# Kernel optimization log

Hardware: AMD Instinct MI355X
Metric: run time of the kernel (lower is better)

The kernel has to match this reference:

```python
import jax, jax.numpy as jnp
import numpy as np
from functools import partial

T, N, E, F_IN, H, F_OUT, L = 12, 20000, 320000, 128, 256, 128, 2


def _agg(feat, src, dst, n):
    # copy_u('x','m') + sum('m','h_N'): for each dst node, sum src-node features
    return jax.ops.segment_sum(feat[src], dst, num_segments=n)


def setup_inputs() -> dict:
    key = jax.random.key(0)
    ks = jax.random.split(key, 16)
    sc = 0.05
    inp = {
        "x": jax.random.normal(ks[0], (T, N, F_IN), jnp.float32),
        "h0": jax.random.normal(ks[1], (L, N, H), jnp.float32),
        "src": jax.random.randint(ks[2], (E,), 0, N, jnp.int32),
        "dst": jax.random.randint(ks[3], (E,), 0, N, jnp.int32),
        # layer 0: x-nets map F_IN->H, h-nets map H->H; stacked [r, u, c]
        "Wx0": jax.random.normal(ks[4], (3, F_IN, H), jnp.float32) * sc,
        "bx0": jnp.zeros((3, H), jnp.float32),
        "Wh0": jax.random.normal(ks[5], (3, H, H), jnp.float32) * sc,
        "bh0": jnp.zeros((3, H), jnp.float32),
        # layer 1: both map H->H
        "Wx1": jax.random.normal(ks[6], (3, H, H), jnp.float32) * sc,
        "bx1": jnp.zeros((3, H), jnp.float32),
        "Wh1": jax.random.normal(ks[7], (3, H, H), jnp.float32) * sc,
        "bh1": jnp.zeros((3, H), jnp.float32),
        "Wo": jax.random.normal(ks[8], (H, F_OUT), jnp.float32) * sc,
        "bo": jnp.zeros((F_OUT,), jnp.float32),
    }
    return inp


def _gru_cell(x_agg, h, Wx, bx, Wh, bh, src, dst, n):
    # reuse_msg_passing=True: h_agg computed once, shared by r_h_net and u_h_net
    h_agg = _agg(h, src, dst, n)
    r = jax.nn.sigmoid(x_agg @ Wx[0] + bx[0] + h_agg @ Wh[0] + bh[0])
    u = jax.nn.sigmoid(x_agg @ Wx[1] + bx[1] + h_agg @ Wh[1] + bh[1])
    # c_h_net runs on r*h, so it needs its own aggregation
    c = jnp.tanh(x_agg @ Wx[2] + bx[2] + _agg(r * h, src, dst, n) @ Wh[2] + bh[2])
    return u * h + (1.0 - u) * c


def reference(x, h0, src, dst, Wx0, bx0, Wh0, bh0, Wx1, bx1, Wh1, bh1, Wo, bo):
    n = h0.shape[1]
    # merge_time_steps=True: aggregate all time steps of x in one pass
    x_aggs = jax.vmap(lambda xi: _agg(xi, src, dst, n))(x)  # [T, N, F_IN]

    def step(carry, x_agg_t):
        h_0, h_1 = carry
        nh0 = _gru_cell(x_agg_t, h_0, Wx0, bx0, Wh0, bh0, src, dst, n)
        nh1 = _gru_cell(_agg(nh0, src, dst, n), h_1, Wx1, bx1, Wh1, bh1, src, dst, n)
        return (nh0, nh1), nh1 @ Wo + bo

    (hf0, hf1), outputs = jax.lax.scan(step, (h0[0], h0[1]), x_aggs)
    return outputs, jnp.stack([hf0, hf1])  # [T,N,F_OUT], [L,N,H]
```

## Files before the change

### kernel.cpp

```cpp
#include <hip/hip_runtime.h>
#include <hip/hip_bf16.h>
#include <stdint.h>

#define T_STEPS 12
#define NN 20000
#define NE 320000
#define FIN 128
#define HD 256
#define FOUT 128
#define PADR 96

typedef __attribute__((ext_vector_type(4))) float f32x4;
typedef __attribute__((ext_vector_type(8))) _Float16 f16x8;

static __device__ __forceinline__ float sigmoidf_(float x) {
  return 1.0f / (1.0f + __expf(-x));
}
static __device__ __forceinline__ float tanhf_(float x) {
  return 1.0f - 2.0f / (__expf(2.0f * x) + 1.0f);
}
static __device__ __forceinline__ ushort f2h(float f) {
  union { ushort s; _Float16 h; } v; v.h = (_Float16)f; return v.s;
}

static __device__ __forceinline__ void gload_lds16(const _Float16* g, _Float16* l) {
  auto gp = (const __attribute__((address_space(1))) _Float16*)g;
  auto lp = (__attribute__((address_space(3))) _Float16*)l;
  __builtin_amdgcn_global_load_lds(gp, lp, 16, 0, 0);
}

__global__ void count_kernel(const int* __restrict__ dst, int* __restrict__ counts) {
  int e = blockIdx.x * blockDim.x + threadIdx.x;
  if (e < NE) atomicAdd(&counts[dst[e]], 1);
}

__global__ void scan_kernel(const int* __restrict__ counts, int* __restrict__ offs,
                            int* __restrict__ cursor) {
  __shared__ int sm[1024];
  __shared__ int carry_s;
  if (threadIdx.x == 0) carry_s = 0;
  __syncthreads();
  const int n = NN;
  int nch = (n + 1023) >> 10;
  for (int c = 0; c < nch; ++c) {
    int i = (c << 10) + (int)threadIdx.x;
    int v = (i < n) ? counts[i] : 0;
    sm[threadIdx.x] = v;
    __syncthreads();
    for (int off = 1; off < 1024; off <<= 1) {
      int t = (threadIdx.x >= (unsigned)off) ? sm[threadIdx.x - off] : 0;
      __syncthreads();
      sm[threadIdx.x] += t;
      __syncthreads();
    }
    int incl = sm[threadIdx.x];
    int carry_local = carry_s;
    if (i < n) {
      int excl = carry_local + incl - v;
      offs[i] = excl;
      cursor[i] = excl;
    }
    __syncthreads();
    if (threadIdx.x == 1023) carry_s = carry_local + incl;
    __syncthreads();
  }
  if (threadIdx.x == 0) offs[n] = carry_s;
}

__global__ void fill_kernel(const int* __restrict__ src, const int* __restrict__ dst,
                            int* __restrict__ cursor, int* __restrict__ esrc) {
  int e = blockIdx.x * blockDim.x + threadIdx.x;
  if (e < NE) {
    int d = dst[e];
    int pos = atomicAdd(&cursor[d], 1);
    esrc[pos] = src[e];
  }
}

static __device__ __forceinline__ void agg_body256(int blk, const float* __restrict__ feat,
                                                   const int* __restrict__ offs,
                                                   const int* __restrict__ esrc,
                                                   _Float16* __restrict__ out) {
  int d = blk * 4 + (threadIdx.x >> 6);
  int lane = threadIdx.x & 63;
  int beg = offs[d], end = offs[d + 1];
  float a[8][4] = {};
  int e = beg;
  for (; e + 7 < end; e += 8) {
    int s[8];
#pragma unroll
    for (int u = 0; u < 8; ++u) s[u] = __builtin_amdgcn_readfirstlane(esrc[e + u]);
#pragma unroll
    for (int u = 0; u < 8; ++u) {
      float4 v = *reinterpret_cast<const float4*>(feat + (size_t)s[u] * 256 + lane * 4);
      a[u][0] += v.x; a[u][1] += v.y; a[u][2] += v.z; a[u][3] += v.w;
    }
  }
  for (; e + 3 < end; e += 4) {
    int s[4];
#pragma unroll
    for (int u = 0; u < 4; ++u) s[u] = __builtin_amdgcn_readfirstlane(esrc[e + u]);
#pragma unroll
    for (int u = 0; u < 4; ++u) {
      float4 v = *reinterpret_cast<const float4*>(feat + (size_t)s[u] * 256 + lane * 4);
      a[u][0] += v.x; a[u][1] += v.y; a[u][2] += v.z; a[u][3] += v.w;
    }
  }
  for (; e < end; ++e) {
    int s0 = __builtin_amdgcn_readfirstlane(esrc[e]);
    float4 v = *reinterpret_cast<const float4*>(feat + (size_t)s0 * 256 + lane * 4);
    a[0][0] += v.x; a[0][1] += v.y; a[0][2] += v.z; a[0][3] += v.w;
  }
  ushort hi[4], lo[4];
#pragma unroll
  for (int p = 0; p < 4; ++p) {
    float s = ((a[0][p] + a[1][p]) + (a[2][p] + a[3][p])) +
              ((a[4][p] + a[5][p]) + (a[6][p] + a[7][p]));
    hi[p] = f2h(s);
    union { ushort us; _Float16 h; } u; u.us = hi[p];
    lo[p] = f2h(s - (float)u.h);
  }
  *reinterpret_cast<ushort4*>(out + (size_t)d * 512 + lane * 4) = *reinterpret_cast<ushort4*>(hi);
  *reinterpret_cast<ushort4*>(out + (size_t)d * 512 + 256 + lane * 4) = *reinterpret_cast<ushort4*>(lo);
}

__global__ void agg_split_h(const float* __restrict__ feat, const int* __restrict__ offs,
                            const int* __restrict__ esrc, _Float16* __restrict__ out) {
  agg_body256(blockIdx.x, feat, offs, esrc, out);
}

__global__ void agg_dual(const float* __restrict__ f0, _Float16* __restrict__ o0,
                         const float* __restrict__ f1, _Float16* __restrict__ o1,
                         const int* __restrict__ offs, const int* __restrict__ esrc) {
  if (blockIdx.y == 0) agg_body256(blockIdx.x, f0, offs, esrc, o0);
  else                 agg_body256(blockIdx.x, f1, offs, esrc, o1);
}

__global__ void agg_split_x(const float* __restrict__ x, const int* __restrict__ offs,
                            const int* __restrict__ esrc, _Float16* __restrict__ out) {
  int t = blockIdx.y;
  const float* feat = x + (size_t)t * NN * FIN;
  _Float16* o = out + (size_t)t * NN * 256;
  int d = blockIdx.x * 4 + (threadIdx.x >> 6);
  int lane = threadIdx.x & 63;
  int beg = offs[d], end = offs[d + 1];
  float a[8][2] = {};
  int e = beg;
  for (; e + 7 < end; e += 8) {
    int s[8];
#pragma unroll
    for (int u = 0; u < 8; ++u) s[u] = __builtin_amdgcn_readfirstlane(esrc[e + u]);
#pragma unroll
    for (int u = 0; u < 8; ++u) {
      float2 v = *reinterpret_cast<const float2*>(feat + (size_t)s[u] * FIN + lane * 2);
      a[u][0] += v.x; a[u][1] += v.y;
    }
  }
  for (; e + 3 < end; e += 4) {
    int s[4];
#pragma unroll
    for (int u = 0; u < 4; ++u) s[u] = __builtin_amdgcn_readfirstlane(esrc[e + u]);
#pragma unroll
    for (int u = 0; u < 4; ++u) {
      float2 v = *reinterpret_cast<const float2*>(feat + (size_t)s[u] * FIN + lane * 2);
      a[u][0] += v.x; a[u][1] += v.y;
    }
  }
  for (; e < end; ++e) {
    int s0 = __builtin_amdgcn_readfirstlane(esrc[e]);
    float2 v = *reinterpret_cast<const float2*>(feat + (size_t)s0 * FIN + lane * 2);
    a[0][0] += v.x; a[0][1] += v.y;
  }
  float s0 = ((a[0][0] + a[1][0]) + (a[2][0] + a[3][0])) +
             ((a[4][0] + a[5][0]) + (a[6][0] + a[7][0]));
  float s1 = ((a[0][1] + a[1][1]) + (a[2][1] + a[3][1])) +
             ((a[4][1] + a[5][1]) + (a[6][1] + a[7][1]));
  ushort2 hi, lo;
  hi.x = f2h(s0); hi.y = f2h(s1);
  union { ushort s; _Float16 h; } u0, u1;
  u0.s = hi.x; u1.s = hi.y;
  lo.x = f2h(s0 - (float)u0.h); lo.y = f2h(s1 - (float)u1.h);
  *reinterpret_cast<ushort2*>(o + (size_t)d * 256 + lane * 2) = hi;
  *reinterpret_cast<ushort2*>(o + (size_t)d * 256 + FIN + lane * 2) = lo;
}

struct GemmP {
  const _Float16* Aa; int lda_a, wrapA, lenA;
  const _Float16* Ab; int lda_b, wrapB;
  const _Float16* B; int ldb;
  float* C; int ldc;
  const float* bias;
  const float* Cacc;
  int M, K, mode;
  float* h; _Float16* hf; float* rh;
  int nch, rpg;
};

static __device__ __forceinline__ void gemm_body(int p, const GemmP& g,
                                                 _Float16* As, _Float16* Bs) {
  int xcd = p & 7;
  int q = p >> 3;
  int rowt = xcd * g.rpg + q / g.nch;
  int chunk = q % g.nch;
  int m0 = rowt * 128;
  if (m0 >= g.M) return;
  int n0 = chunk * 128;

  int tid = threadIdx.x;
  int wave = tid >> 6;
  int lane = tid & 63;
  int wm = wave >> 1, wn = wave & 1;
  int lrow = lane & 15;
  int kgrp = lane >> 4;

  f32x4 acc[4][4] = {};

  int row8 = lane >> 3;
  int swz8 = 8 * ((lane & 7) ^ row8);
  int wrow = wave * 32;

  for (int k0 = 0; k0 < g.K; k0 += 64) {
    const _Float16* Abase;
    int ka, ldA;
    if (k0 < g.lenA) {
      ka = (k0 >= g.wrapA) ? k0 - g.wrapA : k0;
      Abase = g.Aa; ldA = g.lda_a;
    } else {
      int kp = k0 - g.lenA;
      ka = (kp >= g.wrapB) ? kp - g.wrapB : kp;
      Abase = g.Ab; ldA = g.lda_b;
    }
    __syncthreads();
#pragma unroll
    for (int p4 = 0; p4 < 4; ++p4) {
      int r = wrow + p4 * 8;
      gload_lds16(&Abase[(size_t)(m0 + r + row8) * ldA + ka + swz8], &As[r * 64]);
      gload_lds16(&g.B[(size_t)(n0 + r + row8) * g.ldb + k0 + swz8], &Bs[r * 64]);
    }
    __syncthreads();

#pragma unroll
    for (int kk = 0; kk < 2; ++kk) {
      f16x8 af[4], bf[4];
      int kbyte = kk * 64 + kgrp * 16;
#pragma unroll
      for (int i = 0; i < 4; ++i) {
        int ar = wm * 64 + i * 16 + lrow;
        af[i] = *reinterpret_cast<const f16x8*>(
            reinterpret_cast<const char*>(As) + ar * 128 + (kbyte ^ ((ar & 7) << 4)));
        int br = wn * 64 + i * 16 + lrow;
        bf[i] = *reinterpret_cast<const f16x8*>(
            reinterpret_cast<const char*>(Bs) + br * 128 + (kbyte ^ ((br & 7) << 4)));
      }
#pragma unroll
      for (int i = 0; i < 4; ++i)
#pragma unroll
        for (int j = 0; j < 4; ++j)
          acc[i][j] = __builtin_amdgcn_mfma_f32_16x16x32_f16(bf[j], af[i], acc[i][j], 0, 0, 0);
    }
  }

#pragma unroll
  for (int i = 0; i < 4; ++i) {
    int m = m0 + wm * 64 + i * 16 + lrow;
    if (m >= g.M) continue;
#pragma unroll
    for (int j = 0; j < 4; ++j) {
      int colbase = n0 + wn * 64 + j * 16 + kgrp * 4;
      f32x4 v = acc[i][j];
      if (g.mode == 0) {
        float4 bv4 = *reinterpret_cast<const float4*>(&g.bias[colbase]);
        v[0] += bv4.x; v[1] += bv4.y; v[2] += bv4.z; v[3] += bv4.w;
        *reinterpret_cast<f32x4*>(&g.C[(size_t)m * g.ldc + colbase]) = v;
      } else if (g.mode == 1) {
        if (g.Cacc) {
          float4 a4 = *reinterpret_cast<const float4*>(&g.Cacc[(size_t)m * g.ldc + colbase]);
          v[0] += a4.x; v[1] += a4.y; v[2] += a4.z; v[3] += a4.w;
        } else {
          float4 bv4 = *reinterpret_cast<const float4*>(&g.bias[colbase]);
          v[0] += bv4.x; v[1] += bv4.y; v[2] += bv4.z; v[3] += bv4.w;
        }
        if (colbase < 256) {
          float4 hv = *reinterpret_cast<const float4*>(&g.h[(size_t)m * 256 + colbase]);
          f32x4 rv;
          rv[0] = sigmoidf_(v[0]) * hv.x;
          rv[1] = sigmoidf_(v[1]) * hv.y;
          rv[2] = sigmoidf_(v[2]) * hv.z;
          rv[3] = sigmoidf_(v[3]) * hv.w;
          *reinterpret_cast<f32x4*>(&g.rh[(size_t)m * 256 + colbase]) = rv;
        } else if (colbase < 512) {
          v[0] = sigmoidf_(v[0]); v[1] = sigmoidf_(v[1]);
          v[2] = sigmoidf_(v[2]); v[3] = sigmoidf_(v[3]);
          *reinterpret_cast<f32x4*>(&g.C[(size_t)m * g.ldc + colbase]) = v;
        } else {
          *reinterpret_cast<f32x4*>(&g.C[(size_t)m * g.ldc + colbase]) = v;
        }
      } else {
        float4 xc = *reinterpret_cast<const float4*>(&g.C[(size_t)m * g.ldc + 512 + colbase]);
        float4 uu = *reinterpret_cast<const float4*>(&g.C[(size_t)m * g.ldc + 256 + colbase]);
        float* hp = &g.h[(size_t)m * 256 + colbase];
        float4 hv = *reinterpret_cast<const float4*>(hp);
        float4 nh;
        nh.x = uu.x * hv.x + (1.f - uu.x) * tanhf_(xc.x + v[0]);
        nh.y = uu.y * hv.y + (1.f - uu.y) * tanhf_(xc.y + v[1]);
        nh.z = uu.z * hv.z + (1.f - uu.z) * tanhf_(xc.z + v[2]);
        nh.w = uu.w * hv.w + (1.f - uu.w) * tanhf_(xc.w + v[3]);
        *reinterpret_cast<float4*>(hp) = nh;
        if (g.hf) {
          ushort4 hv16;
          hv16.x = f2h(nh.x); hv16.y = f2h(nh.y);
          hv16.z = f2h(nh.z); hv16.w = f2h(nh.w);
          *reinterpret_cast<ushort4*>(&g.hf[(size_t)m * 256 + colbase]) = hv16;
        }
      }
    }
  }
}

__global__ __launch_bounds__(256) void combo(GemmP ga, int na, GemmP gb, int nb, GemmP gc) {
  __shared__ _Float16 As[128 * 64];
  __shared__ _Float16 Bs[128 * 64];
  int b = blockIdx.x;
  int sel = (b < na) ? 0 : ((b < na + nb) ? 1 : 2);
  int idx = b - ((sel > 0) ? na : 0) - ((sel > 1) ? nb : 0);
  GemmP g = (sel == 0) ? ga : ((sel == 1) ? gb : gc);
  gemm_body(idx, g, As, Bs);
}

__global__ void wtrans(const float* __restrict__ W, _Float16* __restrict__ dst,
                       int K, int ldw, int ldd, int koff, int mode) {
  int k = blockIdx.x * blockDim.x + threadIdx.x;
  int n = blockIdx.y;
  if (k < K) {
    float w = W[(size_t)k * ldw + n];
    _Float16 hi = (_Float16)w;
    dst[(size_t)n * ldd + koff + k] = mode ? (_Float16)(w - (float)hi) : hi;
  }
}

__global__ void bias_comb(const float* __restrict__ bx, const float* __restrict__ bh,
                          float* __restrict__ out) {
  int i = blockIdx.x * blockDim.x + threadIdx.x;
  if (i < 768) out[i] = bx[i] + bh[i];
}

__global__ void copy_kernel(const float* __restrict__ in, float* __restrict__ out, int n4) {
  int i = blockIdx.x * blockDim.x + threadIdx.x;
  if (i < n4) reinterpret_cast<float4*>(out)[i] = reinterpret_cast<const float4*>(in)[i];
}

extern "C" void kernel_launch(void* const* d_in, const int* in_sizes, int n_in,
                              void* d_out, int out_size, void* d_ws, size_t ws_size,
                              hipStream_t stream) {
  const float* x   = (const float*)d_in[0];
  const float* h0  = (const float*)d_in[1];
  const int*   src = (const int*)d_in[2];
  const int*   dst = (const int*)d_in[3];
  const float* Wx0 = (const float*)d_in[4];
  const float* bx0 = (const float*)d_in[5];
  const float* Wh0 = (const float*)d_in[6];
  const float* bh0 = (const float*)d_in[7];
  const float* Wx1 = (const float*)d_in[8];
  const float* bx1 = (const float*)d_in[9];
  const float* Wh1 = (const float*)d_in[10];
  const float* bh1 = (const float*)d_in[11];
  const float* Wo  = (const float*)d_in[12];
  const float* bo  = (const float*)d_in[13];
  float* out = (float*)d_out;

  char* p = (char*)d_ws;
  auto alloc = [&](size_t bytes) {
    char* r = p;
    p += (bytes + 255) & ~(size_t)255;
    return r;
  };
  int* offs   = (int*)alloc((NN + 1) * sizeof(int));
  int* cursor = (int*)alloc(NN * sizeof(int));
  int* counts = (int*)alloc(NN * sizeof(int));
  int* esrc   = (int*)alloc(NE * sizeof(int));
  _Float16* B0  = (_Float16*)alloc((size_t)768 * 1152 * 2);
  _Float16* B0h = (_Float16*)alloc((size_t)256 * 768 * 2);
  _Float16* B1  = (_Float16*)alloc((size_t)768 * 1536 * 2);
  _Float16* B1h = (_Float16*)alloc((size_t)256 * 768 * 2);
  _Float16* Bo  = (_Float16*)alloc((size_t)128 * 256 * 2);
  float* b0c  = (float*)alloc(768 * 4);
  float* b1c  = (float*)alloc(768 * 4);
  _Float16* XAGG  = (_Float16*)alloc(((size_t)T_STEPS * NN + PADR) * 256 * 2);
  _Float16* H0AGG = (_Float16*)alloc((size_t)(NN + PADR) * 512 * 2);
  _Float16* H1AGG = (_Float16*)alloc((size_t)(NN + PADR) * 512 * 2);
  _Float16* RHAGG = (_Float16*)alloc((size_t)(NN + PADR) * 512 * 2);
  _Float16* h1f   = (_Float16*)alloc((size_t)(NN + PADR) * 256 * 2);
  float* rhf  = (float*)alloc((size_t)NN * 256 * 4);
  float* xw0  = (float*)alloc((size_t)NN * 768 * 4);
  float* xw1  = (float*)alloc((size_t)NN * 768 * 4);

  float* h0c = out + (size_t)T_STEPS * NN * FOUT;
  float* h1c = h0c + (size_t)NN * HD;

  hipMemsetAsync(counts, 0, NN * sizeof(int), stream);
  count_kernel<<<(NE + 255) / 256, 256, 0, stream>>>(dst, counts);
  scan_kernel<<<1, 1024, 0, stream>>>(counts, offs, cursor);
  fill_kernel<<<(NE + 255) / 256, 256, 0, stream>>>(src, dst, cursor, esrc);

  hipMemsetAsync(B0, 0, (size_t)768 * 1152 * 2, stream);
  hipMemsetAsync(B1, 0, (size_t)768 * 1536 * 2, stream);
  for (int g = 0; g < 3; ++g) {
    const float* W = Wx0 + (size_t)g * 128 * 256;
    _Float16* D = B0 + (size_t)g * 256 * 1152;
    wtrans<<<dim3(1, 256), 256, 0, stream>>>(W, D, 128, 256, 1152, 0, 0);
    wtrans<<<dim3(1, 256), 256, 0, stream>>>(W, D, 128, 256, 1152, 128, 0);
    wtrans<<<dim3(1, 256), 256, 0, stream>>>(W, D, 128, 256, 1152, 256, 1);
  }
  for (int g = 0; g < 2; ++g) {
    const float* W = Wh0 + (size_t)g * 256 * 256;
    _Float16* D = B0 + (size_t)g * 256 * 1152;
    wtrans<<<dim3(1, 256), 256, 0, stream>>>(W, D, 256, 256, 1152, 384, 0);
    wtrans<<<dim3(1, 256), 256, 0, stream>>>(W, D, 256, 256, 1152, 640, 0);
    wtrans<<<dim3(1, 256), 256, 0, stream>>>(W, D, 256, 256, 1152, 896, 1);
  }
  {
    const float* W = Wh0 + (size_t)2 * 256 * 256;
    wtrans<<<dim3(1, 256), 256, 0, stream>>>(W, B0h, 256, 256, 768, 0, 0);
    wtrans<<<dim3(1, 256), 256, 0, stream>>>(W, B0h, 256, 256, 768, 256, 0);
    wtrans<<<dim3(1, 256), 256, 0, stream>>>(W, B0h, 256, 256, 768, 512, 1);
  }
  for (int g = 0; g < 3; ++g) {
    const float* W = Wx1 + (size_t)g * 256 * 256;
    _Float16* D = B1 + (size_t)g * 256 * 1536;
    wtrans<<<dim3(1, 256), 256, 0, stream>>>(W, D, 256, 256, 1536, 0, 0);
    wtrans<<<dim3(1, 256), 256, 0, stream>>>(W, D, 256, 256, 1536, 256, 0);
    wtrans<<<dim3(1, 256), 256, 0, stream>>>(W, D, 256, 256, 1536, 512, 1);
  }
  for (int g = 0; g < 2; ++g) {
    const float* W = Wh1 + (size_t)g * 256 * 256;
    _Float16* D = B1 + (size_t)g * 256 * 1536;
    wtrans<<<dim3(1, 256), 256, 0, stream>>>(W, D, 256, 256, 1536, 768, 0);
    wtrans<<<dim3(1, 256), 256, 0, stream>>>(W, D, 256, 256, 1536, 1024, 0);
    wtrans<<<dim3(1, 256), 256, 0, stream>>>(W, D, 256, 256, 1536, 1280, 1);
  }
  {
    const float* W = Wh1 + (size_t)2 * 256 * 256;
    wtrans<<<dim3(1, 256), 256, 0, stream>>>(W, B1h, 256, 256, 768, 0, 0);
    wtrans<<<dim3(1, 256), 256, 0, stream>>>(W, B1h, 256, 256, 768, 256, 0);
    wtrans<<<dim3(1, 256), 256, 0, stream>>>(W, B1h, 256, 256, 768, 512, 1);
  }
  wtrans<<<dim3(1, 128), 256, 0, stream>>>(Wo, Bo, 256, 128, 256, 0, 0);
  bias_comb<<<3, 256, 0, stream>>>(bx0, bh0, b0c);
  bias_comb<<<3, 256, 0, stream>>>(bx1, bh1, b1c);

  copy_kernel<<<(2 * NN * HD / 4 + 255) / 256, 256, 0, stream>>>(h0, h0c, 2 * NN * HD / 4);

  dim3 blk(256);
  const int RPG = 20;
  int g6 = 8 * RPG * 6, g2 = 8 * RPG * 2, g1 = 8 * RPG * 1;
  int agg_grid = NN / 4;

  agg_split_x<<<dim3(agg_grid, T_STEPS), blk, 0, stream>>>(x, offs, esrc, XAGG);
  agg_split_h<<<agg_grid, blk, 0, stream>>>(h0c, offs, esrc, H0AGG);

  GemmP dummy = {};
  dummy.nch = 1; dummy.rpg = 1;

  for (int t = 0; t < T_STEPS; ++t) {
    GemmP C1p = {RHAGG, 512, 512, 768, nullptr, 0, 0, B1h, 768, xw1, 768, nullptr, nullptr,
                 NN, 768, 2, h1c, h1f, nullptr, 2, RPG};
    GemmP L0p = {XAGG + (size_t)t * NN * 256, 256, 256, 384, H0AGG, 512, 512,
                 B0, 1152, xw0, 768, b0c, nullptr, NN, 1152, 1, h0c, nullptr, rhf, 6, RPG};
    if (t == 0)
      combo<<<g6, blk, 0, stream>>>(L0p, g6, dummy, 0, dummy);
    else
      combo<<<g2 + g6, blk, 0, stream>>>(C1p, g2, L0p, g6, dummy);

    agg_dual<<<dim3(agg_grid, 2), blk, 0, stream>>>(rhf, RHAGG, h1c, H1AGG, offs, esrc);

    GemmP C0p = {RHAGG, 512, 512, 768, nullptr, 0, 0, B0h, 768, xw0, 768, nullptr, nullptr,
                 NN, 768, 2, h0c, nullptr, nullptr, 2, RPG};
    GemmP L1a = {H1AGG, 512, 512, 768, nullptr, 0, 0, B1 + 768, 1536, xw1, 768, b1c, nullptr,
                 NN, 768, 0, nullptr, nullptr, nullptr, 6, RPG};
    combo<<<g2 + g6, blk, 0, stream>>>(C0p, g2, L1a, g6, dummy);

    agg_split_h<<<agg_grid, blk, 0, stream>>>(h0c, offs, esrc, H0AGG);

    GemmP L1b = {H0AGG, 512, 512, 768, nullptr, 0, 0, B1, 1536, xw1, 768, nullptr, xw1,
                 NN, 768, 1, h1c, nullptr, rhf, 6, RPG};
    GemmP OPp = {h1f, 256, 256, 256, nullptr, 0, 0, Bo, 256,
                 out + (size_t)(t > 0 ? t - 1 : 0) * NN * FOUT, FOUT, bo, nullptr,
                 NN, 256, 0, nullptr, nullptr, nullptr, 1, RPG};
    if (t == 0)
      combo<<<g6, blk, 0, stream>>>(L1b, g6, dummy, 0, dummy);
    else
      combo<<<g6 + g1, blk, 0, stream>>>(L1b, g6, OPp, g1, dummy);

    agg_split_h<<<agg_grid, blk, 0, stream>>>(rhf, offs, esrc, RHAGG);
  }

  GemmP C1f = {RHAGG, 512, 512, 768, nullptr, 0, 0, B1h, 768, xw1, 768, nullptr, nullptr,
               NN, 768, 2, h1c, h1f, nullptr, 2, RPG};
  combo<<<g2, blk, 0, stream>>>(C1f, g2, dummy, 0, dummy);
  GemmP OPl = {h1f, 256, 256, 256, nullptr, 0, 0, Bo, 256,
               out + (size_t)(T_STEPS - 1) * NN * FOUT, FOUT, bo, nullptr,
               NN, 256, 0, nullptr, nullptr, nullptr, 1, RPG};
  combo<<<g1, blk, 0, stream>>>(OPl, g1, dummy, 0, dummy);
}
```

Baseline: 4.813 ms.

## Gather fp16 node features in aggregation instead of fp32

The per-edge gather kernels now read fp16 copies of h0, h1 and r*h instead of fp32 rows, with fp32 accumulation kept. The GRU epilogue writes r*h directly as fp16 and the C0 gemm also emits an fp16 copy of h0, which removes half the gather bandwidth in the memory-bound aggregation steps. The cost is lower precision of the aggregated inputs (fp16 rounding per source row), though the hi/lo split output is kept.

```diff
diff --git a/kernel.cpp b/kernel.cpp
--- a/kernel.cpp
+++ b/kernel.cpp
@@ -21,6 +21,9 @@
 }
 static __device__ __forceinline__ ushort f2h(float f) {
   union { ushort s; _Float16 h; } v; v.h = (_Float16)f; return v.s;
+}
+static __device__ __forceinline__ float h2f(ushort u) {
+  union { ushort s; _Float16 h; } v; v.s = u; return (float)v.h;
 }
 
 static __device__ __forceinline__ void gload_lds16(const _Float16* g, _Float16* l) {
@@ -77,10 +80,10 @@
   }
 }
 
-static __device__ __forceinline__ void agg_body256(int blk, const float* __restrict__ feat,
-                                                   const int* __restrict__ offs,
-                                                   const int* __restrict__ esrc,
-                                                   _Float16* __restrict__ out) {
+static __device__ __forceinline__ void agg_body256_f16(int blk, const _Float16* __restrict__ feat,
+                                                       const int* __restrict__ offs,
+                                                       const int* __restrict__ esrc,
+                                                       _Float16* __restrict__ out) {
   int d = blk * 4 + (threadIdx.x >> 6);
   int lane = threadIdx.x & 63;
   int beg = offs[d], end = offs[d + 1];
@@ -92,8 +95,8 @@
     for (int u = 0; u < 8; ++u) s[u] = __builtin_amdgcn_readfirstlane(esrc[e + u]);
 #pragma unroll
     for (int u = 0; u < 8; ++u) {
-      float4 v = *reinterpret_cast<const float4*>(feat + (size_t)s[u] * 256 + lane * 4);
-      a[u][0] += v.x; a[u][1] += v.y; a[u][2] += v.z; a[u][3] += v.w;
+      ushort4 v = *reinterpret_cast<const ushort4*>(feat + (size_t)s[u] * 256 + lane * 4);
+      a[u][0] += h2f(v.x); a[u][1] += h2f(v.y); a[u][2] += h2f(v.z); a[u][3] += h2f(v.w);
     }
   }
   for (; e + 3 < end; e += 4) {
@@ -102,14 +105,14 @@
     for (int u = 0; u < 4; ++u) s[u] = __builtin_amdgcn_readfirstlane(esrc[e + u]);
 #pragma unroll
     for (int u = 0; u < 4; ++u) {
-      float4 v = *reinterpret_cast<const float4*>(feat + (size_t)s[u] * 256 + lane * 4);
-      a[u][0] += v.x; a[u][1] += v.y; a[u][2] += v.z; a[u][3] += v.w;
+      ushort4 v = *reinterpret_cast<const ushort4*>(feat + (size_t)s[u] * 256 + lane * 4);
+      a[u][0] += h2f(v.x); a[u][1] += h2f(v.y); a[u][2] += h2f(v.z); a[u][3] += h2f(v.w);
     }
   }
   for (; e < end; ++e) {
     int s0 = __builtin_amdgcn_readfirstlane(esrc[e]);
-    float4 v = *reinterpret_cast<const float4*>(feat + (size_t)s0 * 256 + lane * 4);
-    a[0][0] += v.x; a[0][1] += v.y; a[0][2] += v.z; a[0][3] += v.w;
+    ushort4 v = *reinterpret_cast<const ushort4*>(feat + (size_t)s0 * 256 + lane * 4);
+    a[0][0] += h2f(v.x); a[0][1] += h2f(v.y); a[0][2] += h2f(v.z); a[0][3] += h2f(v.w);
   }
   ushort hi[4], lo[4];
 #pragma unroll
@@ -124,16 +127,16 @@
   *reinterpret_cast<ushort4*>(out + (size_t)d * 512 + 256 + lane * 4) = *reinterpret_cast<ushort4*>(lo);
 }
 
-__global__ void agg_split_h(const float* __restrict__ feat, const int* __restrict__ offs,
-                            const int* __restrict__ esrc, _Float16* __restrict__ out) {
-  agg_body256(blockIdx.x, feat, offs, esrc, out);
-}
-
-__global__ void agg_dual(const float* __restrict__ f0, _Float16* __restrict__ o0,
-                         const float* __restrict__ f1, _Float16* __restrict__ o1,
-                         const int* __restrict__ offs, const int* __restrict__ esrc) {
-  if (blockIdx.y == 0) agg_body256(blockIdx.x, f0, offs, esrc, o0);
-  else                 agg_body256(blockIdx.x, f1, offs, esrc, o1);
+__global__ void agg_h16(const _Float16* __restrict__ feat, const int* __restrict__ offs,
+                        const int* __restrict__ esrc, _Float16* __restrict__ out) {
+  agg_body256_f16(blockIdx.x, feat, offs, esrc, out);
+}
+
+__global__ void agg_dual16(const _Float16* __restrict__ f0, _Float16* __restrict__ o0,
+                           const _Float16* __restrict__ f1, _Float16* __restrict__ o1,
+                           const int* __restrict__ offs, const int* __restrict__ esrc) {
+  if (blockIdx.y == 0) agg_body256_f16(blockIdx.x, f0, offs, esrc, o0);
+  else                 agg_body256_f16(blockIdx.x, f1, offs, esrc, o1);
 }
 
 __global__ void agg_split_x(const float* __restrict__ x, const int* __restrict__ offs,
@@ -192,7 +195,7 @@
   const float* bias;
   const float* Cacc;
   int M, K, mode;
-  float* h; _Float16* hf; float* rh;
+  float* h; _Float16* hf; _Float16* rh16;
   int nch, rpg;
 };
 
@@ -282,12 +285,12 @@
         }
         if (colbase < 256) {
           float4 hv = *reinterpret_cast<const float4*>(&g.h[(size_t)m * 256 + colbase]);
-          f32x4 rv;
-          rv[0] = sigmoidf_(v[0]) * hv.x;
-          rv[1] = sigmoidf_(v[1]) * hv.y;
-          rv[2] = sigmoidf_(v[2]) * hv.z;
-          rv[3] = sigmoidf_(v[3]) * hv.w;
-          *reinterpret_cast<f32x4*>(&g.rh[(size_t)m * 256 + colbase]) = rv;
+          ushort4 rv;
+          rv.x = f2h(sigmoidf_(v[0]) * hv.x);
+          rv.y = f2h(sigmoidf_(v[1]) * hv.y);
+          rv.z = f2h(sigmoidf_(v[2]) * hv.z);
+          rv.w = f2h(sigmoidf_(v[3]) * hv.w);
+          *reinterpret_cast<ushort4*>(&g.rh16[(size_t)m * 256 + colbase]) = rv;
         } else if (colbase < 512) {
           v[0] = sigmoidf_(v[0]); v[1] = sigmoidf_(v[1]);
           v[2] = sigmoidf_(v[2]); v[3] = sigmoidf_(v[3]);
@@ -349,6 +352,15 @@
   if (i < n4) reinterpret_cast<float4*>(out)[i] = reinterpret_cast<const float4*>(in)[i];
 }
 
+__global__ void cvt16(const float* __restrict__ in, _Float16* __restrict__ out, int n4) {
+  int i = blockIdx.x * blockDim.x + threadIdx.x;
+  if (i >= n4) return;
+  float4 v = reinterpret_cast<const float4*>(in)[i];
+  ushort4 o;
+  o.x = f2h(v.x); o.y = f2h(v.y); o.z = f2h(v.z); o.w = f2h(v.w);
+  reinterpret_cast<ushort4*>(out)[i] = o;
+}
+
 extern "C" void kernel_launch(void* const* d_in, const int* in_sizes, int n_in,
                               void* d_out, int out_size, void* d_ws, size_t ws_size,
                               hipStream_t stream) {
@@ -389,8 +401,9 @@
   _Float16* H0AGG = (_Float16*)alloc((size_t)(NN + PADR) * 512 * 2);
   _Float16* H1AGG = (_Float16*)alloc((size_t)(NN + PADR) * 512 * 2);
   _Float16* RHAGG = (_Float16*)alloc((size_t)(NN + PADR) * 512 * 2);
+  _Float16* h0f   = (_Float16*)alloc((size_t)(NN + PADR) * 256 * 2);
   _Float16* h1f   = (_Float16*)alloc((size_t)(NN + PADR) * 256 * 2);
-  float* rhf  = (float*)alloc((size_t)NN * 256 * 4);
+  _Float16* rhf16 = (_Float16*)alloc((size_t)(NN + PADR) * 256 * 2);
   float* xw0  = (float*)alloc((size_t)NN * 768 * 4);
   float* xw1  = (float*)alloc((size_t)NN * 768 * 4);
 
@@ -449,6 +462,8 @@
   bias_comb<<<3, 256, 0, stream>>>(bx1, bh1, b1c);
 
   copy_kernel<<<(2 * NN * HD / 4 + 255) / 256, 256, 0, stream>>>(h0, h0c, 2 * NN * HD / 4);
+  cvt16<<<(NN * HD / 4 + 255) / 256, 256, 0, stream>>>(h0, h0f, NN * HD / 4);
+  cvt16<<<(NN * HD / 4 + 255) / 256, 256, 0, stream>>>(h0 + (size_t)NN * HD, h1f, NN * HD / 4);
 
   dim3 blk(256);
   const int RPG = 20;
@@ -456,7 +471,7 @@
   int agg_grid = NN / 4;
 
   agg_split_x<<<dim3(agg_grid, T_STEPS), blk, 0, stream>>>(x, offs, esrc, XAGG);
-  agg_split_h<<<agg_grid, blk, 0, stream>>>(h0c, offs, esrc, H0AGG);
+  agg_h16<<<agg_grid, blk, 0, stream>>>(h0f, offs, esrc, H0AGG);
 
   GemmP dummy = {};
   dummy.nch = 1; dummy.rpg = 1;
@@ -465,24 +480,24 @@
     GemmP C1p = {RHAGG, 512, 512, 768, nullptr, 0, 0, B1h, 768, xw1, 768, nullptr, nullptr,
                  NN, 768, 2, h1c, h1f, nullptr, 2, RPG};
     GemmP L0p = {XAGG + (size_t)t * NN * 256, 256, 256, 384, H0AGG, 512, 512,
-                 B0, 1152, xw0, 768, b0c, nullptr, NN, 1152, 1, h0c, nullptr, rhf, 6, RPG};
+                 B0, 1152, xw0, 768, b0c, nullptr, NN, 1152, 1, h0c, nullptr, rhf16, 6, RPG};
     if (t == 0)
       combo<<<g6, blk, 0, stream>>>(L0p, g6, dummy, 0, dummy);
     else
       combo<<<g2 + g6, blk, 0, stream>>>(C1p, g2, L0p, g6, dummy);
 
-    agg_dual<<<dim3(agg_grid, 2), blk, 0, stream>>>(rhf, RHAGG, h1c, H1AGG, offs, esrc);
+    agg_dual16<<<dim3(agg_grid, 2), blk, 0, stream>>>(rhf16, RHAGG, h1f, H1AGG, offs, esrc);
 
     GemmP C0p = {RHAGG, 512, 512, 768, nullptr, 0, 0, B0h, 768, xw0, 768, nullptr, nullptr,
-                 NN, 768, 2, h0c, nullptr, nullptr, 2, RPG};
+                 NN, 768, 2, h0c, h0f, nullptr, 2, RPG};
     GemmP L1a = {H1AGG, 512, 512, 768, nullptr, 0, 0, B1 + 768, 1536, xw1, 768, b1c, nullptr,
                  NN, 768, 0, nullptr, nullptr, nullptr, 6, RPG};
     combo<<<g2 + g6, blk, 0, stream>>>(C0p, g2, L1a, g6, dummy);
 
-    agg_split_h<<<agg_grid, blk, 0, stream>>>(h0c, offs, esrc, H0AGG);
+    agg_h16<<<agg_grid, blk, 0, stream>>>(h0f, offs, esrc, H0AGG);
 
     GemmP L1b = {H0AGG, 512, 512, 768, nullptr, 0, 0, B1, 1536, xw1, 768, nullptr, xw1,
-                 NN, 768, 1, h1c, nullptr, rhf, 6, RPG};
+                 NN, 768, 1, h1c, nullptr, rhf16, 6, RPG};
     GemmP OPp = {h1f, 256, 256, 256, nullptr, 0, 0, Bo, 256,
                  out + (size_t)(t > 0 ? t - 1 : 0) * NN * FOUT, FOUT, bo, nullptr,
                  NN, 256, 0, nullptr, nullptr, nullptr, 1, RPG};
@@ -491,7 +506,7 @@
     else
       combo<<<g6 + g1, blk, 0, stream>>>(L1b, g6, OPp, g1, dummy);
 
-    agg_split_h<<<agg_grid, blk, 0, stream>>>(rhf, offs, esrc, RHAGG);
+    agg_h16<<<agg_grid, blk, 0, stream>>>(rhf16, offs, esrc, RHAGG);
   }
 
   GemmP C1f = {RHAGG, 512, 512, 768, nullptr, 0, 0, B1h, 768, xw1, 768, nullptr, nullptr,
```

Measured after the change: 4.190 ms. -13.0%, faster.
